# Kernel tuning notes

Hardware: AMD Instinct MI355X
Metric: run time of the kernel (lower is better)

## Reference

```python
import jax, jax.numpy as jnp
import numpy as np

B, T = 64, 256
E = 300          # embedding_size
H = 512          # hidden_num
L = 9            # label_size
V = 30000        # vocab_size
S = 30000        # sentence_size


def setup_inputs() -> dict:
    key = jax.random.key(0)
    ks = jax.random.split(key, 14)
    D = 2 * E
    inp = {
        "text": jax.random.randint(ks[0], (B, T), 0, V, dtype=jnp.int32),
        "sentence": jax.random.randint(ks[1], (B, T), 0, S, dtype=jnp.int32),
        "labels": jax.random.randint(ks[2], (B, T), 0, L, dtype=jnp.int32),
        "word_emb": jax.random.normal(ks[3], (V, E), jnp.float32) * 0.05,
        "sent_emb": jax.random.normal(ks[4], (S, E), jnp.float32) * 0.05,
        "Wk_f": jax.random.normal(ks[5], (D, 4 * H), jnp.float32) / np.sqrt(D).astype(np.float32),
        "Wr_f": jax.random.normal(ks[6], (H, 4 * H), jnp.float32) / np.sqrt(H).astype(np.float32),
        "b_f": jnp.zeros((4 * H,), jnp.float32),
        "Wk_b": jax.random.normal(ks[7], (D, 4 * H), jnp.float32) / np.sqrt(D).astype(np.float32),
        "Wr_b": jax.random.normal(ks[8], (H, 4 * H), jnp.float32) / np.sqrt(H).astype(np.float32),
        "b_b": jnp.zeros((4 * H,), jnp.float32),
        "Wd": jax.random.normal(ks[9], (2 * H, L), jnp.float32) / np.sqrt(2 * H).astype(np.float32),
        "bd": jnp.zeros((L,), jnp.float32),
        "trans": jax.random.uniform(ks[10], (L, L), jnp.float32),
    }
    return inp


def lstm(x, Wk, Wr, b):
    # x: [B,T,D]; Keras LSTM gate order i,f,g,o; sigmoid recurrent act, tanh act.
    xz = jnp.einsum('btd,dk->btk', x, Wk) + b  # one big GEMM for all timesteps
    h0 = jnp.zeros((x.shape[0], Wr.shape[0]), x.dtype)

    def step(carry, z_t):
        h, c = carry
        z = z_t + h @ Wr
        i, f, g, o = jnp.split(z, 4, axis=-1)
        c = jax.nn.sigmoid(f) * c + jax.nn.sigmoid(i) * jnp.tanh(g)
        h = jax.nn.sigmoid(o) * jnp.tanh(c)
        return (h, c), h

    _, hs = jax.lax.scan(step, (h0, h0), jnp.swapaxes(xz, 0, 1))
    return jnp.swapaxes(hs, 0, 1)  # [B,T,H]


def crf_log_likelihood(logits, labels, mask, trans):
    maskf = mask.astype(logits.dtype)
    # unary score of the gold path
    unary = jnp.take_along_axis(logits, labels[..., None], axis=-1)[..., 0]  # [B,T]
    unary = jnp.sum(unary * maskf, axis=-1)
    # binary (transition) score
    binary = trans[labels[:, :-1], labels[:, 1:]]  # [B,T-1]
    binary = jnp.sum(binary * maskf[:, 1:], axis=-1)
    # forward algorithm (log partition), masked steps carry alpha
    logits_tm = jnp.swapaxes(logits, 0, 1)  # [T,B,L]
    mask_tm = jnp.swapaxes(mask, 0, 1)

    def step(alpha, inputs):
        logit_t, m_t = inputs
        new = jax.nn.logsumexp(alpha[:, :, None] + trans[None], axis=1) + logit_t
        return jnp.where(m_t[:, None], new, alpha), None

    alpha, _ = jax.lax.scan(step, logits_tm[0], (logits_tm[1:], mask_tm[1:]))
    log_norm = jax.nn.logsumexp(alpha, axis=-1)
    return unary + binary - log_norm


def crf_decode(logits, trans, mask):
    b, t, l = logits.shape
    logits_tm = jnp.swapaxes(logits, 0, 1)
    mask_tm = jnp.swapaxes(mask, 0, 1)
    ident = jnp.broadcast_to(jnp.arange(l)[None], (b, l))

    def step(alpha, inputs):
        logit_t, m_t = inputs
        score = alpha[:, :, None] + trans[None]      # [B,L,L]
        bp = jnp.argmax(score, axis=1)               # [B,L]
        new = jnp.max(score, axis=1) + logit_t
        alpha = jnp.where(m_t[:, None], new, alpha)
        bp = jnp.where(m_t[:, None], bp, ident)      # identity through padding
        return alpha, bp

    alpha, bps = jax.lax.scan(step, logits_tm[0], (logits_tm[1:], mask_tm[1:]))
    last = jnp.argmax(alpha, axis=-1)  # [B]

    def back(tag, bp):
        prev = jnp.take_along_axis(bp, tag[:, None], axis=1)[:, 0]
        return prev, prev

    _, tags = jax.lax.scan(back, last, bps, reverse=True)  # [T-1,B], original time order
    tags = jnp.concatenate([tags, last[None]], axis=0)     # [T,B]
    return jnp.swapaxes(tags, 0, 1).astype(jnp.int32)


def reference(text, sentence, labels, word_emb, sent_emb, Wk_f, Wr_f, b_f,
              Wk_b, Wr_b, b_b, Wd, bd, trans):
    x = jnp.concatenate([word_emb[text], sent_emb[sentence]], axis=-1)  # [B,T,2E]
    hf = lstm(x, Wk_f, Wr_f, b_f)
    hb = lstm(x[:, ::-1], Wk_b, Wr_b, b_b)[:, ::-1]
    h = jnp.concatenate([hf, hb], axis=-1)  # [B,T,2H]
    logits = h @ Wd + bd                    # [B,T,L]
    text_lens = jnp.sum((text != 0).astype(jnp.int32), axis=-1)
    mask = jnp.arange(T)[None, :] < text_lens[:, None]
    log_likelihood = crf_log_likelihood(logits, labels, mask, trans)
    pred_tags = crf_decode(logits, trans, mask)
    return logits, text_lens, log_likelihood, pred_tags
```

## Files before the change

kernel.cpp:

```cpp
#include <hip/hip_runtime.h>
#include <hip/hip_bf16.h>
#include <math.h>

#define BB 64
#define TT 256
#define EE 300
#define DD 600
#define KP 608
#define HH 512
#define G4 2048
#define LL 9
#define NT (BB*TT)

typedef __attribute__((ext_vector_type(8))) short short8;
typedef __attribute__((ext_vector_type(4))) float floatx4;

#define XZF_OFF  ((size_t)0)
#define XZ_BYTES ((size_t)NT * G4 * 2)
#define XZB_OFF  (XZF_OFF + XZ_BYTES)
#define HSR_OFF  (XZB_OFF + XZ_BYTES)
#define HS_BYTES ((size_t)NT * HH * 2)
#define HSF_OFF  (HSR_OFF)
#define HSB_OFF  (HSR_OFF + HS_BYTES)
#define XG_OFF   (HSR_OFF)
#define WKT_OFF  (HSR_OFF + 19922944)
#define BP_OFF   (HSR_OFF + 25165824)
#define WRT_OFF  (HSR_OFF + (size_t)2 * HS_BYTES)
#define HB_OFF   (WRT_OFF + 4194304)
#define HB_BYTES ((size_t)2 * 2 * BB * HH * 4)
#define LEN_OFF  (HB_OFF + HB_BYTES)

#define OUT_LOGITS 0
#define OUT_LENS   (BB*TT*LL)
#define OUT_LL     (OUT_LENS + BB)
#define OUT_TAGS   (OUT_LL + BB)

__global__ __launch_bounds__(256) void prep_xg(
    const int* __restrict__ text, const int* __restrict__ sent,
    const float* __restrict__ wemb, const float* __restrict__ semb,
    __hip_bfloat16* __restrict__ xg)
{
    int n = blockIdx.x;
    int ti = text[n], si = sent[n];
    __hip_bfloat16* o = xg + (size_t)n * KP;
    for (int k = threadIdx.x; k < KP; k += 256) {
        float v = 0.f;
        if (k < EE)      v = wemb[(size_t)ti * EE + k];
        else if (k < DD) v = semb[(size_t)si * EE + (k - EE)];
        o[k] = __float2bfloat16(v);
    }
}

__global__ __launch_bounds__(256) void transpose_w(
    const float* __restrict__ Wf, const float* __restrict__ Wb,
    __hip_bfloat16* __restrict__ outT, int Din, int Dpad)
{
    int dir = blockIdx.z;
    const float* W = dir ? Wb : Wf;
    __hip_bfloat16* o = outT + (size_t)dir * G4 * Dpad;
    int n0 = blockIdx.x * 64, d0 = blockIdx.y * 64;
    __shared__ float tile[64][65];
    int c = threadIdx.x & 63, r4 = threadIdx.x >> 6;
    #pragma unroll
    for (int rr = 0; rr < 64; rr += 4) {
        int d = d0 + rr + r4;
        tile[rr + r4][c] = (d < Din) ? W[(size_t)d * G4 + n0 + c] : 0.f;
    }
    __syncthreads();
    #pragma unroll
    for (int rr = 0; rr < 64; rr += 4) {
        int n = n0 + rr + r4;
        int d = d0 + c;
        if (d < Dpad) o[(size_t)n * Dpad + d] = __float2bfloat16(tile[c][rr + r4]);
    }
}

__global__ __launch_bounds__(256) void embed_gemm(
    const __hip_bfloat16* __restrict__ xg,
    const __hip_bfloat16* __restrict__ WkT,
    const float* __restrict__ b_f, const float* __restrict__ b_b,
    __hip_bfloat16* __restrict__ xz_f, __hip_bfloat16* __restrict__ xz_b)
{
    int dir = blockIdx.z;
    const __hip_bfloat16* wt = WkT + (size_t)dir * G4 * KP;
    const float* bias = dir ? b_b : b_f;
    __hip_bfloat16* xz = dir ? xz_b : xz_f;

    int n0 = blockIdx.x * 64;
    int c0 = blockIdx.y * 64;
    int wave = threadIdx.x >> 6, lane = threadIdx.x & 63;
    int mt2 = (wave & 1) * 2;
    int nt2 = (wave >> 1) * 2;
    int lm = lane & 15, lk8 = (lane >> 4) * 8;

    const short8* ap[2], *bp[2];
    ap[0] = (const short8*)(xg + (size_t)(n0 + (mt2+0)*16 + lm) * KP + lk8);
    ap[1] = (const short8*)(xg + (size_t)(n0 + (mt2+1)*16 + lm) * KP + lk8);
    bp[0] = (const short8*)(wt + (size_t)(c0 + (nt2+0)*16 + lm) * KP + lk8);
    bp[1] = (const short8*)(wt + (size_t)(c0 + (nt2+1)*16 + lm) * KP + lk8);

    floatx4 acc[2][2] = {};
    for (int kc = 0; kc < KP/32; ++kc) {
        short8 a0 = ap[0][kc*4];
        short8 a1 = ap[1][kc*4];
        short8 b0 = bp[0][kc*4];
        short8 b1 = bp[1][kc*4];
        acc[0][0] = __builtin_amdgcn_mfma_f32_16x16x32_bf16(a0, b0, acc[0][0], 0,0,0);
        acc[0][1] = __builtin_amdgcn_mfma_f32_16x16x32_bf16(a0, b1, acc[0][1], 0,0,0);
        acc[1][0] = __builtin_amdgcn_mfma_f32_16x16x32_bf16(a1, b0, acc[1][0], 0,0,0);
        acc[1][1] = __builtin_amdgcn_mfma_f32_16x16x32_bf16(a1, b1, acc[1][1], 0,0,0);
    }

    float bias0 = bias[c0 + (nt2+0)*16 + lm];
    float bias1 = bias[c0 + (nt2+1)*16 + lm];
    int lr = (lane >> 4) * 4;
    #pragma unroll
    for (int mi = 0; mi < 2; ++mi)
        #pragma unroll
        for (int ni = 0; ni < 2; ++ni) {
            int col = c0 + (nt2+ni)*16 + lm;
            float bs = ni ? bias1 : bias0;
            #pragma unroll
            for (int r = 0; r < 4; ++r) {
                int row = n0 + (mt2+mi)*16 + lr + r;
                xz[(size_t)row * G4 + col] = __float2bfloat16(acc[mi][ni][r] + bs);
            }
        }
}

__global__ __launch_bounds__(256, 1) void lstm_coop(
    const __hip_bfloat16* __restrict__ xz_f, const __hip_bfloat16* __restrict__ xz_b,
    const __hip_bfloat16* __restrict__ WrT,
    unsigned* __restrict__ hbx,
    __hip_bfloat16* __restrict__ hs_f, __hip_bfloat16* __restrict__ hs_b)
{
    int blk = blockIdx.x;
    int dir = blk >> 7, sub = blk & 127;
    int r0 = (sub >> 5) * 16;
    int h0 = (sub & 31) * 16;
    int tid = threadIdx.x;
    int gate = tid >> 6, lane = tid & 63;
    int lm = lane & 15, lk8 = (lane >> 4) * 8;

    const __hip_bfloat16* xz = dir ? xz_b : xz_f;
    __hip_bfloat16* hs = dir ? hs_b : hs_f;
    const __hip_bfloat16* wrt = WrT + (size_t)dir * G4 * HH;
    unsigned* hbd = hbx + (size_t)dir * 2 * BB * HH;

    short8 bfrag[16];
    {
        const short8* wp = (const short8*)(wrt + (size_t)(gate*HH + h0 + lm) * HH + lk8);
        #pragma unroll
        for (int kc = 0; kc < 16; ++kc) bfrag[kc] = wp[kc*4];
    }

    __shared__ unsigned short htile[16][520];
    __shared__ float zbuf[4][16][17];

    int er = tid >> 3, ec = (tid & 7) * 2;
    float c0st = 0.f, c1st = 0.f;

    int zr = (lane >> 4) * 4;

    for (int t = 0; t < TT; ++t) {
        int tok = dir ? (TT - 1 - t) : t;

        float xzv[4];
        #pragma unroll
        for (int r = 0; r < 4; ++r) {
            int n = (r0 + zr + r) * TT + tok;
            xzv[r] = __bfloat162float(xz[(size_t)n * G4 + gate*HH + h0 + lm]);
        }

        unsigned long long v[16];
        {
            const unsigned long long* src = (const unsigned long long*)
                (hbd + (size_t)(t & 1) * BB * HH + (size_t)r0 * HH);
            const unsigned long long pat =
                ((unsigned long long)(unsigned)t << 48) |
                ((unsigned long long)(unsigned)t << 16);
            for (;;) {
                #pragma unroll
                for (int q = 0; q < 16; ++q)
                    v[q] = __hip_atomic_load(src + tid + 256*q,
                            __ATOMIC_RELAXED, __HIP_MEMORY_SCOPE_AGENT);
                unsigned long long bad = 0;
                #pragma unroll
                for (int q = 0; q < 16; ++q)
                    bad |= (v[q] ^ pat) & 0xFFFF0000FFFF0000ULL;
                if (bad == 0) break;
                __builtin_amdgcn_s_sleep(2);
            }
        }
        #pragma unroll
        for (int q = 0; q < 16; ++q) {
            int idx = tid + 256*q;
            int row = idx >> 8, cp = idx & 255;
            unsigned lo = (unsigned)(v[q] & 0xffffu);
            unsigned hi = (unsigned)((v[q] >> 32) & 0xffffu);
            *(unsigned*)&htile[row][cp * 2] = lo | (hi << 16);
        }
        __syncthreads();

        floatx4 acc = {};
        #pragma unroll
        for (int kc = 0; kc < 16; ++kc) {
            short8 a = *(const short8*)&htile[lm][kc * 32 + lk8];
            acc = __builtin_amdgcn_mfma_f32_16x16x32_bf16(a, bfrag[kc], acc, 0,0,0);
        }

        #pragma unroll
        for (int r = 0; r < 4; ++r)
            zbuf[gate][zr + r][lm] = acc[r] + xzv[r];
        __syncthreads();

        if (tid < 128) {
            float zi0 = zbuf[0][er][ec],   zi1 = zbuf[0][er][ec+1];
            float zf0 = zbuf[1][er][ec],   zf1 = zbuf[1][er][ec+1];
            float zg0 = zbuf[2][er][ec],   zg1 = zbuf[2][er][ec+1];
            float zo0 = zbuf[3][er][ec],   zo1 = zbuf[3][er][ec+1];
            float si0 = 1.f/(1.f+__expf(-zi0)), si1 = 1.f/(1.f+__expf(-zi1));
            float sf0 = 1.f/(1.f+__expf(-zf0)), sf1 = 1.f/(1.f+__expf(-zf1));
            float so0 = 1.f/(1.f+__expf(-zo0)), so1 = 1.f/(1.f+__expf(-zo1));
            c0st = sf0 * c0st + si0 * tanhf(zg0);
            c1st = sf1 * c1st + si1 * tanhf(zg1);
            float h0v = so0 * tanhf(c0st);
            float h1v = so1 * tanhf(c1st);
            unsigned u0 = (unsigned)__builtin_bit_cast(unsigned short, __float2bfloat16(h0v));
            unsigned u1 = (unsigned)__builtin_bit_cast(unsigned short, __float2bfloat16(h1v));
            unsigned tg = (unsigned)(t + 1) << 16;
            unsigned long long pay =
                ((unsigned long long)(tg | u1) << 32) | (unsigned long long)(tg | u0);
            __hip_atomic_store(
                (unsigned long long*)(hbd + (size_t)((t+1) & 1) * BB * HH
                                          + (size_t)(r0 + er) * HH + h0 + ec),
                pay, __ATOMIC_RELAXED, __HIP_MEMORY_SCOPE_AGENT);
            *(unsigned*)(hs + ((size_t)(r0 + er) * TT + tok) * HH + h0 + ec) =
                u0 | (u1 << 16);
        }
    }
}

__global__ __launch_bounds__(64) void logits_kernel(
    const __hip_bfloat16* __restrict__ hs_f, const __hip_bfloat16* __restrict__ hs_b,
    const float* __restrict__ Wd, const float* __restrict__ bd,
    float* __restrict__ out)
{
    int n = blockIdx.x;
    int tid = threadIdx.x;
    __shared__ float red[64][10];
    float acc[LL] = {};
    for (int kk = 0; kk < 16; ++kk) {
        int k = kk * 64 + tid;
        float hv = (k < HH) ? __bfloat162float(hs_f[(size_t)n * HH + k])
                            : __bfloat162float(hs_b[(size_t)n * HH + (k - HH)]);
        const float* w = Wd + (size_t)k * LL;
        #pragma unroll
        for (int l = 0; l < LL; ++l) acc[l] += hv * w[l];
    }
    #pragma unroll
    for (int l = 0; l < LL; ++l) red[tid][l] = acc[l];
    __syncthreads();
    for (int s = 32; s > 0; s >>= 1) {
        if (tid < s)
            for (int l = 0; l < LL; ++l) red[tid][l] += red[tid + s][l];
        __syncthreads();
    }
    if (tid < LL) out[(size_t)n * LL + tid] = red[0][tid] + bd[tid];
}

__global__ __launch_bounds__(256) void lens_kernel(
    const int* __restrict__ text, float* __restrict__ out_lens, int* __restrict__ len_i)
{
    int b = blockIdx.x, tid = threadIdx.x;
    __shared__ int sred[256];
    sred[tid] = (text[b * TT + tid] != 0) ? 1 : 0;
    __syncthreads();
    for (int s = 128; s > 0; s >>= 1) {
        if (tid < s) sred[tid] += sred[tid + s];
        __syncthreads();
    }
    if (tid == 0) { out_lens[b] = (float)sred[0]; len_i[b] = sred[0]; }
}

__global__ __launch_bounds__(128) void crf_kernel(
    const float* __restrict__ logits, const int* __restrict__ labels,
    const float* __restrict__ trans, const int* __restrict__ len_i,
    int* __restrict__ bp, float* __restrict__ out_ll, float* __restrict__ out_tags)
{
    int b = blockIdx.x, tid = threadIdx.x;
    int len = len_i[b];
    const float* lg = logits + (size_t)b * TT * LL;
    const int* lab = labels + b * TT;

    __shared__ float tr[81];
    __shared__ float alpha[LL], vit[LL], newa[LL], newv[LL];
    __shared__ int newbp[LL];
    __shared__ float partial[128];

    if (tid < 81) tr[tid] = trans[tid];
    if (tid < LL) { alpha[tid] = lg[tid]; vit[tid] = lg[tid]; }
    __syncthreads();

    float up = 0.f;
    for (int t = tid; t < TT; t += 128) {
        float m = (t < len) ? 1.f : 0.f;
        up += m * lg[t * LL + lab[t]];
        if (t >= 1) up += m * tr[lab[t - 1] * LL + lab[t]];
    }
    partial[tid] = up;
    __syncthreads();
    for (int s = 64; s > 0; s >>= 1) {
        if (tid < s) partial[tid] += partial[tid + s];
        __syncthreads();
    }

    for (int t = 1; t < TT; ++t) {
        bool m = t < len;
        if (tid < LL) {
            int j = tid;
            float mx = -1e30f;
            #pragma unroll
            for (int i = 0; i < LL; ++i) mx = fmaxf(mx, alpha[i] + tr[i * LL + j]);
            float s = 0.f;
            #pragma unroll
            for (int i = 0; i < LL; ++i) s += __expf(alpha[i] + tr[i * LL + j] - mx);
            newa[j] = mx + __logf(s) + lg[t * LL + j];
        } else if (tid >= 64 && tid < 64 + LL) {
            int j = tid - 64;
            float best = -1e30f; int bi = 0;
            #pragma unroll
            for (int i = 0; i < LL; ++i) {
                float sc = vit[i] + tr[i * LL + j];
                if (sc > best) { best = sc; bi = i; }
            }
            newv[j] = best + lg[t * LL + j];
            newbp[j] = bi;
        }
        __syncthreads();
        if (tid < LL) {
            if (m) alpha[tid] = newa[tid];
        } else if (tid >= 64 && tid < 64 + LL) {
            int j = tid - 64;
            if (m) vit[j] = newv[j];
            bp[((size_t)b * (TT - 1) + (t - 1)) * LL + j] = m ? newbp[j] : j;
        }
        __syncthreads();
    }

    if (tid == 0) {
        float mx = -1e30f;
        #pragma unroll
        for (int j = 0; j < LL; ++j) mx = fmaxf(mx, alpha[j]);
        float s = 0.f;
        #pragma unroll
        for (int j = 0; j < LL; ++j) s += __expf(alpha[j] - mx);
        out_ll[b] = partial[0] - (mx + __logf(s));

        float bv = vit[0]; int last = 0;
        #pragma unroll
        for (int j = 1; j < LL; ++j) if (vit[j] > bv) { bv = vit[j]; last = j; }
        out_tags[b * TT + (TT - 1)] = (float)last;
        int tag = last;
        for (int s2 = TT - 2; s2 >= 0; --s2) {
            tag = bp[((size_t)b * (TT - 1) + s2) * LL + tag];
            out_tags[b * TT + s2] = (float)tag;
        }
    }
}

extern "C" void kernel_launch(void* const* d_in, const int* in_sizes, int n_in,
                              void* d_out, int out_size, void* d_ws, size_t ws_size,
                              hipStream_t stream)
{
    const int*   text  = (const int*)d_in[0];
    const int*   sent  = (const int*)d_in[1];
    const int*   labels= (const int*)d_in[2];
    const float* wemb  = (const float*)d_in[3];
    const float* semb  = (const float*)d_in[4];
    const float* Wk_f  = (const float*)d_in[5];
    const float* Wr_f  = (const float*)d_in[6];
    const float* b_f   = (const float*)d_in[7];
    const float* Wk_b  = (const float*)d_in[8];
    const float* Wr_b  = (const float*)d_in[9];
    const float* b_b   = (const float*)d_in[10];
    const float* Wd    = (const float*)d_in[11];
    const float* bd    = (const float*)d_in[12];
    const float* trans = (const float*)d_in[13];
    float* out = (float*)d_out;

    char* ws = (char*)d_ws;
    __hip_bfloat16* xz_f = (__hip_bfloat16*)(ws + XZF_OFF);
    __hip_bfloat16* xz_b = (__hip_bfloat16*)(ws + XZB_OFF);
    __hip_bfloat16* hs_f = (__hip_bfloat16*)(ws + HSF_OFF);
    __hip_bfloat16* hs_b = (__hip_bfloat16*)(ws + HSB_OFF);
    __hip_bfloat16* xg   = (__hip_bfloat16*)(ws + XG_OFF);
    __hip_bfloat16* WkT  = (__hip_bfloat16*)(ws + WKT_OFF);
    __hip_bfloat16* WrT  = (__hip_bfloat16*)(ws + WRT_OFF);
    unsigned*       hbx  = (unsigned*)(ws + HB_OFF);
    int*      bp    = (int*)(ws + BP_OFF);
    int*      leni  = (int*)(ws + LEN_OFF);

    prep_xg <<<NT,  256, 0, stream>>>(text, sent, wemb, semb, xg);
    transpose_w<<<dim3(G4/64, (KP+63)/64, 2), 256, 0, stream>>>(Wk_f, Wk_b, WkT, DD, KP);
    transpose_w<<<dim3(G4/64, HH/64, 2),      256, 0, stream>>>(Wr_f, Wr_b, WrT, HH, HH);
    hipMemsetAsync(ws + HB_OFF, 0, HB_BYTES + 256, stream);

    embed_gemm<<<dim3(NT/64, G4/64, 2), 256, 0, stream>>>(
        xg, WkT, b_f, b_b, xz_f, xz_b);

    {
        void* args[] = { (void*)&xz_f, (void*)&xz_b, (void*)&WrT,
                         (void*)&hbx, (void*)&hs_f, (void*)&hs_b };
        hipLaunchCooperativeKernel((const void*)lstm_coop, dim3(256), dim3(256),
                                   args, 0, stream);
    }

    logits_kernel<<<NT, 64, 0, stream>>>(hs_f, hs_b, Wd, bd, out + OUT_LOGITS);
    lens_kernel<<<BB, 256, 0, stream>>>(text, out + OUT_LENS, leni);
    crf_kernel<<<BB, 128, 0, stream>>>(out + OUT_LOGITS, labels, trans, leni,
                                       bp, out + OUT_LL, out + OUT_TAGS);
}
```

Before: 1.578 ms.

## Add volatile fast-path exchange to LSTM, MFMA logits, fused warp-level CRF

Remaps LSTM blocks so each batch-row group spreads across XCDs by block index, and adds a volatile (non-atomic) fast exchange buffer for the recurrent h that is polled first. After repeated misses it falls back to the existing agent-scope atomic buffer. Widens the embedding GEMM tile to 128 rows per block. Replaces the scalar logits reduction with an MFMA kernel over a bf16-transposed Wd. Fuses lens and CRF into one kernel that keeps logits, transitions and backpointers in LDS and does the forward and Viterbi recursion with wave shuffles instead of block syncs. The volatile path relies on cache coherence behaviour that the code does not guarantee, which adds a correctness risk.

```diff
diff --git a/kernel.cpp b/kernel.cpp
--- a/kernel.cpp
+++ b/kernel.cpp
@@ -24,11 +24,11 @@
 #define HSB_OFF  (HSR_OFF + HS_BYTES)
 #define XG_OFF   (HSR_OFF)
 #define WKT_OFF  (HSR_OFF + 19922944)
-#define BP_OFF   (HSR_OFF + 25165824)
 #define WRT_OFF  (HSR_OFF + (size_t)2 * HS_BYTES)
-#define HB_OFF   (WRT_OFF + 4194304)
-#define HB_BYTES ((size_t)2 * 2 * BB * HH * 4)
-#define LEN_OFF  (HB_OFF + HB_BYTES)
+#define BK_OFF   (WRT_OFF + 4194304)
+#define FAST_OFF (BK_OFF + 524288)
+#define EX_BYTES ((size_t)2 * 2 * BB * HH * 4)
+#define WDT_OFF  XZF_OFF
 
 #define OUT_LOGITS 0
 #define OUT_LENS   (BB*TT*LL)
@@ -75,6 +75,15 @@
     }
 }
 
+__global__ __launch_bounds__(256) void prep_wdT(
+    const float* __restrict__ Wd, __hip_bfloat16* __restrict__ WdT)
+{
+    for (int i = threadIdx.x + blockIdx.x * 256; i < 16 * 1024; i += gridDim.x * 256) {
+        int nn = i >> 10, k = i & 1023;
+        WdT[i] = __float2bfloat16(nn < LL ? Wd[(size_t)k * LL + nn] : 0.f);
+    }
+}
+
 __global__ __launch_bounds__(256) void embed_gemm(
     const __hip_bfloat16* __restrict__ xg,
     const __hip_bfloat16* __restrict__ WkT,
@@ -86,58 +95,64 @@
     const float* bias = dir ? b_b : b_f;
     __hip_bfloat16* xz = dir ? xz_b : xz_f;
 
-    int n0 = blockIdx.x * 64;
+    int n0 = blockIdx.x * 128;
     int c0 = blockIdx.y * 64;
     int wave = threadIdx.x >> 6, lane = threadIdx.x & 63;
-    int mt2 = (wave & 1) * 2;
-    int nt2 = (wave >> 1) * 2;
+    int m0 = (wave & 1) * 64;
+    int nn0 = (wave >> 1) * 32;
     int lm = lane & 15, lk8 = (lane >> 4) * 8;
 
-    const short8* ap[2], *bp[2];
-    ap[0] = (const short8*)(xg + (size_t)(n0 + (mt2+0)*16 + lm) * KP + lk8);
-    ap[1] = (const short8*)(xg + (size_t)(n0 + (mt2+1)*16 + lm) * KP + lk8);
-    bp[0] = (const short8*)(wt + (size_t)(c0 + (nt2+0)*16 + lm) * KP + lk8);
-    bp[1] = (const short8*)(wt + (size_t)(c0 + (nt2+1)*16 + lm) * KP + lk8);
-
-    floatx4 acc[2][2] = {};
+    const short8 *ap[4], *bp2[2];
+    #pragma unroll
+    for (int i = 0; i < 4; ++i)
+        ap[i] = (const short8*)(xg + (size_t)(n0 + m0 + i*16 + lm) * KP + lk8);
+    #pragma unroll
+    for (int i = 0; i < 2; ++i)
+        bp2[i] = (const short8*)(wt + (size_t)(c0 + nn0 + i*16 + lm) * KP + lk8);
+
+    floatx4 acc[4][2] = {};
     for (int kc = 0; kc < KP/32; ++kc) {
-        short8 a0 = ap[0][kc*4];
-        short8 a1 = ap[1][kc*4];
-        short8 b0 = bp[0][kc*4];
-        short8 b1 = bp[1][kc*4];
+        short8 a0 = ap[0][kc*4], a1 = ap[1][kc*4], a2 = ap[2][kc*4], a3 = ap[3][kc*4];
+        short8 b0 = bp2[0][kc*4], b1 = bp2[1][kc*4];
         acc[0][0] = __builtin_amdgcn_mfma_f32_16x16x32_bf16(a0, b0, acc[0][0], 0,0,0);
         acc[0][1] = __builtin_amdgcn_mfma_f32_16x16x32_bf16(a0, b1, acc[0][1], 0,0,0);
         acc[1][0] = __builtin_amdgcn_mfma_f32_16x16x32_bf16(a1, b0, acc[1][0], 0,0,0);
         acc[1][1] = __builtin_amdgcn_mfma_f32_16x16x32_bf16(a1, b1, acc[1][1], 0,0,0);
-    }
-
-    float bias0 = bias[c0 + (nt2+0)*16 + lm];
-    float bias1 = bias[c0 + (nt2+1)*16 + lm];
+        acc[2][0] = __builtin_amdgcn_mfma_f32_16x16x32_bf16(a2, b0, acc[2][0], 0,0,0);
+        acc[2][1] = __builtin_amdgcn_mfma_f32_16x16x32_bf16(a2, b1, acc[2][1], 0,0,0);
+        acc[3][0] = __builtin_amdgcn_mfma_f32_16x16x32_bf16(a3, b0, acc[3][0], 0,0,0);
+        acc[3][1] = __builtin_amdgcn_mfma_f32_16x16x32_bf16(a3, b1, acc[3][1], 0,0,0);
+    }
+
     int lr = (lane >> 4) * 4;
     #pragma unroll
-    for (int mi = 0; mi < 2; ++mi)
-        #pragma unroll
-        for (int ni = 0; ni < 2; ++ni) {
-            int col = c0 + (nt2+ni)*16 + lm;
-            float bs = ni ? bias1 : bias0;
+    for (int ni = 0; ni < 2; ++ni) {
+        int col = c0 + nn0 + ni*16 + lm;
+        float bs = bias[col];
+        #pragma unroll
+        for (int mi = 0; mi < 4; ++mi) {
             #pragma unroll
             for (int r = 0; r < 4; ++r) {
-                int row = n0 + (mt2+mi)*16 + lr + r;
+                int row = n0 + m0 + mi*16 + lr + r;
                 xz[(size_t)row * G4 + col] = __float2bfloat16(acc[mi][ni][r] + bs);
             }
         }
+    }
 }
 
 __global__ __launch_bounds__(256, 1) void lstm_coop(
     const __hip_bfloat16* __restrict__ xz_f, const __hip_bfloat16* __restrict__ xz_b,
     const __hip_bfloat16* __restrict__ WrT,
-    unsigned* __restrict__ hbx,
+    unsigned* __restrict__ bk,
+    unsigned* __restrict__ fast,
     __hip_bfloat16* __restrict__ hs_f, __hip_bfloat16* __restrict__ hs_b)
 {
     int blk = blockIdx.x;
-    int dir = blk >> 7, sub = blk & 127;
-    int r0 = (sub >> 5) * 16;
-    int h0 = (sub & 31) * 16;
+    int g = blk & 7;
+    int member = blk >> 3;
+    int dir = g >> 2;
+    int r0 = (g & 3) * 16;
+    int h0 = member * 16;
     int tid = threadIdx.x;
     int gate = tid >> 6, lane = tid & 63;
     int lm = lane & 15, lk8 = (lane >> 4) * 8;
@@ -145,7 +160,8 @@
     const __hip_bfloat16* xz = dir ? xz_b : xz_f;
     __hip_bfloat16* hs = dir ? hs_b : hs_f;
     const __hip_bfloat16* wrt = WrT + (size_t)dir * G4 * HH;
-    unsigned* hbd = hbx + (size_t)dir * 2 * BB * HH;
+    unsigned* bkd = bk + (size_t)dir * 2 * BB * HH;
+    unsigned* fsd = fast + (size_t)dir * 2 * BB * HH;
 
     short8 bfrag[16];
     {
@@ -159,30 +175,41 @@
 
     int er = tid >> 3, ec = (tid & 7) * 2;
     float c0st = 0.f, c1st = 0.f;
-
     int zr = (lane >> 4) * 4;
+
+    bool fastok = true;
+    int fallcnt = 0;
 
     for (int t = 0; t < TT; ++t) {
         int tok = dir ? (TT - 1 - t) : t;
-
-        float xzv[4];
-        #pragma unroll
-        for (int r = 0; r < 4; ++r) {
-            int n = (r0 + zr + r) * TT + tok;
-            xzv[r] = __bfloat162float(xz[(size_t)n * G4 + gate*HH + h0 + lm]);
-        }
+        size_t soff = (size_t)(t & 1) * BB * HH + (size_t)r0 * HH;
+        const unsigned long long pat =
+            ((unsigned long long)(unsigned)t << 48) |
+            ((unsigned long long)(unsigned)t << 16);
 
         unsigned long long v[16];
-        {
-            const unsigned long long* src = (const unsigned long long*)
-                (hbd + (size_t)(t & 1) * BB * HH + (size_t)r0 * HH);
-            const unsigned long long pat =
-                ((unsigned long long)(unsigned)t << 48) |
-                ((unsigned long long)(unsigned)t << 16);
+        bool got = false;
+        if (fastok) {
+            const volatile unsigned long long* fsrc =
+                (const volatile unsigned long long*)(fsd + soff);
+            for (int spin = 0; spin < 24; ++spin) {
+                unsigned long long bad = 0;
+                #pragma unroll
+                for (int q = 0; q < 16; ++q) v[q] = fsrc[tid + 256*q];
+                #pragma unroll
+                for (int q = 0; q < 16; ++q)
+                    bad |= (v[q] ^ pat) & 0xFFFF0000FFFF0000ULL;
+                if (__all(bad == 0)) { got = true; break; }
+                __builtin_amdgcn_s_sleep(1);
+            }
+            if (!got) { if (++fallcnt >= 8) fastok = false; }
+        }
+        if (!got) {
+            const unsigned long long* bsrc = (const unsigned long long*)(bkd + soff);
             for (;;) {
                 #pragma unroll
                 for (int q = 0; q < 16; ++q)
-                    v[q] = __hip_atomic_load(src + tid + 256*q,
+                    v[q] = __hip_atomic_load(bsrc + tid + 256*q,
                             __ATOMIC_RELAXED, __HIP_MEMORY_SCOPE_AGENT);
                 unsigned long long bad = 0;
                 #pragma unroll
@@ -192,13 +219,19 @@
                 __builtin_amdgcn_s_sleep(2);
             }
         }
+
+        float xzv[4];
+        #pragma unroll
+        for (int r = 0; r < 4; ++r) {
+            int n = (r0 + zr + r) * TT + tok;
+            xzv[r] = __bfloat162float(xz[(size_t)n * G4 + gate*HH + h0 + lm]);
+        }
+
         #pragma unroll
         for (int q = 0; q < 16; ++q) {
-            int idx = tid + 256*q;
-            int row = idx >> 8, cp = idx & 255;
             unsigned lo = (unsigned)(v[q] & 0xffffu);
             unsigned hi = (unsigned)((v[q] >> 32) & 0xffffu);
-            *(unsigned*)&htile[row][cp * 2] = lo | (hi << 16);
+            *(unsigned*)&htile[q][tid * 2] = lo | (hi << 16);
         }
         __syncthreads();
 
@@ -231,142 +264,140 @@
             unsigned tg = (unsigned)(t + 1) << 16;
             unsigned long long pay =
                 ((unsigned long long)(tg | u1) << 32) | (unsigned long long)(tg | u0);
-            __hip_atomic_store(
-                (unsigned long long*)(hbd + (size_t)((t+1) & 1) * BB * HH
-                                          + (size_t)(r0 + er) * HH + h0 + ec),
-                pay, __ATOMIC_RELAXED, __HIP_MEMORY_SCOPE_AGENT);
+            size_t eoff = (size_t)((t+1) & 1) * BB * HH + (size_t)(r0 + er) * HH + h0 + ec;
+            *(volatile unsigned long long*)(fsd + eoff) = pay;
+            __hip_atomic_store((unsigned long long*)(bkd + eoff), pay,
+                               __ATOMIC_RELAXED, __HIP_MEMORY_SCOPE_AGENT);
             *(unsigned*)(hs + ((size_t)(r0 + er) * TT + tok) * HH + h0 + ec) =
                 u0 | (u1 << 16);
         }
     }
 }
 
-__global__ __launch_bounds__(64) void logits_kernel(
+__global__ __launch_bounds__(256) void logits_kernel(
     const __hip_bfloat16* __restrict__ hs_f, const __hip_bfloat16* __restrict__ hs_b,
-    const float* __restrict__ Wd, const float* __restrict__ bd,
+    const __hip_bfloat16* __restrict__ WdT, const float* __restrict__ bd,
     float* __restrict__ out)
 {
-    int n = blockIdx.x;
-    int tid = threadIdx.x;
-    __shared__ float red[64][10];
-    float acc[LL] = {};
-    for (int kk = 0; kk < 16; ++kk) {
-        int k = kk * 64 + tid;
-        float hv = (k < HH) ? __bfloat162float(hs_f[(size_t)n * HH + k])
-                            : __bfloat162float(hs_b[(size_t)n * HH + (k - HH)]);
-        const float* w = Wd + (size_t)k * LL;
-        #pragma unroll
-        for (int l = 0; l < LL; ++l) acc[l] += hv * w[l];
-    }
-    #pragma unroll
-    for (int l = 0; l < LL; ++l) red[tid][l] = acc[l];
-    __syncthreads();
-    for (int s = 32; s > 0; s >>= 1) {
-        if (tid < s)
-            for (int l = 0; l < LL; ++l) red[tid][l] += red[tid + s][l];
-        __syncthreads();
-    }
-    if (tid < LL) out[(size_t)n * LL + tid] = red[0][tid] + bd[tid];
-}
-
-__global__ __launch_bounds__(256) void lens_kernel(
-    const int* __restrict__ text, float* __restrict__ out_lens, int* __restrict__ len_i)
+    int n0 = blockIdx.x * 64;
+    int wave = threadIdx.x >> 6, lane = threadIdx.x & 63;
+    int lm = lane & 15, lk8 = (lane >> 4) * 8;
+    int nw = n0 + wave * 16;
+    const short8* af = (const short8*)(hs_f + (size_t)(nw + lm) * HH + lk8);
+    const short8* ab = (const short8*)(hs_b + (size_t)(nw + lm) * HH + lk8);
+    const short8* bw = (const short8*)(WdT + (size_t)lm * 1024 + lk8);
+    floatx4 acc = {};
+    #pragma unroll
+    for (int kc = 0; kc < 16; ++kc) {
+        acc = __builtin_amdgcn_mfma_f32_16x16x32_bf16(af[kc*4], bw[kc*4], acc, 0,0,0);
+        acc = __builtin_amdgcn_mfma_f32_16x16x32_bf16(ab[kc*4], bw[(kc+16)*4], acc, 0,0,0);
+    }
+    if (lm < LL) {
+        float bv = bd[lm];
+        #pragma unroll
+        for (int r = 0; r < 4; ++r) {
+            int n = nw + (lane >> 4) * 4 + r;
+            out[(size_t)n * LL + lm] = acc[r] + bv;
+        }
+    }
+}
+
+__global__ __launch_bounds__(256) void crf_kernel(
+    const float* __restrict__ logits, const int* __restrict__ text,
+    const int* __restrict__ labels, const float* __restrict__ trans,
+    float* __restrict__ out_lens, float* __restrict__ out_ll,
+    float* __restrict__ out_tags)
 {
     int b = blockIdx.x, tid = threadIdx.x;
-    __shared__ int sred[256];
-    sred[tid] = (text[b * TT + tid] != 0) ? 1 : 0;
+    const float* lg = logits + (size_t)b * TT * LL;
+    const int* lab = labels + b * TT;
+
+    __shared__ float lgs[TT * LL];
+    __shared__ float trs[81];
+    __shared__ unsigned char bps[255 * LL + 1];
+    __shared__ float partial[256];
+    __shared__ int ired[256];
+    __shared__ float tagf[TT];
+
+    for (int i = tid; i < TT * LL; i += 256) lgs[i] = lg[i];
+    if (tid < 81) trs[tid] = trans[tid];
+    ired[tid] = (text[b * TT + tid] != 0) ? 1 : 0;
     __syncthreads();
     for (int s = 128; s > 0; s >>= 1) {
-        if (tid < s) sred[tid] += sred[tid + s];
+        if (tid < s) ired[tid] += ired[tid + s];
         __syncthreads();
     }
-    if (tid == 0) { out_lens[b] = (float)sred[0]; len_i[b] = sred[0]; }
-}
-
-__global__ __launch_bounds__(128) void crf_kernel(
-    const float* __restrict__ logits, const int* __restrict__ labels,
-    const float* __restrict__ trans, const int* __restrict__ len_i,
-    int* __restrict__ bp, float* __restrict__ out_ll, float* __restrict__ out_tags)
-{
-    int b = blockIdx.x, tid = threadIdx.x;
-    int len = len_i[b];
-    const float* lg = logits + (size_t)b * TT * LL;
-    const int* lab = labels + b * TT;
-
-    __shared__ float tr[81];
-    __shared__ float alpha[LL], vit[LL], newa[LL], newv[LL];
-    __shared__ int newbp[LL];
-    __shared__ float partial[128];
-
-    if (tid < 81) tr[tid] = trans[tid];
-    if (tid < LL) { alpha[tid] = lg[tid]; vit[tid] = lg[tid]; }
-    __syncthreads();
+    int len = ired[0];
+    if (tid == 0) out_lens[b] = (float)len;
 
     float up = 0.f;
-    for (int t = tid; t < TT; t += 128) {
+    for (int t = tid; t < TT; t += 256) {
         float m = (t < len) ? 1.f : 0.f;
-        up += m * lg[t * LL + lab[t]];
-        if (t >= 1) up += m * tr[lab[t - 1] * LL + lab[t]];
+        up += m * lgs[t * LL + lab[t]];
+        if (t >= 1) up += m * trs[lab[t - 1] * LL + lab[t]];
     }
     partial[tid] = up;
     __syncthreads();
-    for (int s = 64; s > 0; s >>= 1) {
+    for (int s = 128; s > 0; s >>= 1) {
         if (tid < s) partial[tid] += partial[tid + s];
         __syncthreads();
     }
 
-    for (int t = 1; t < TT; ++t) {
-        bool m = t < len;
-        if (tid < LL) {
-            int j = tid;
+    if (tid < 64) {
+        int lane = tid;
+        int j = (lane < LL) ? lane : 0;
+        float trj[LL];
+        #pragma unroll
+        for (int i = 0; i < LL; ++i) trj[i] = trs[i * LL + j];
+        float alpha = lgs[j];
+        float vit = alpha;
+        for (int t = 1; t < TT; ++t) {
+            bool m = t < len;
+            float lgv = lgs[t * LL + j];
+            float ta[LL];
+            float mx = -1e30f, bv = -1e30f; int bi = 0;
+            #pragma unroll
+            for (int i = 0; i < LL; ++i) {
+                float av = __shfl(alpha, i);
+                float vv = __shfl(vit, i);
+                ta[i] = av + trj[i];
+                mx = fmaxf(mx, ta[i]);
+                float sv = vv + trj[i];
+                if (sv > bv) { bv = sv; bi = i; }
+            }
+            float s = 0.f;
+            #pragma unroll
+            for (int i = 0; i < LL; ++i) s += __expf(ta[i] - mx);
+            float newa = mx + __logf(s) + lgv;
+            float newv = bv + lgv;
+            if (m) { alpha = newa; vit = newv; }
+            if (lane < LL) bps[(t - 1) * LL + lane] = (unsigned char)(m ? bi : lane);
+        }
+        float aX[LL], vX[LL];
+        #pragma unroll
+        for (int i = 0; i < LL; ++i) { aX[i] = __shfl(alpha, i); vX[i] = __shfl(vit, i); }
+        if (lane == 0) {
             float mx = -1e30f;
             #pragma unroll
-            for (int i = 0; i < LL; ++i) mx = fmaxf(mx, alpha[i] + tr[i * LL + j]);
+            for (int i = 0; i < LL; ++i) mx = fmaxf(mx, aX[i]);
             float s = 0.f;
             #pragma unroll
-            for (int i = 0; i < LL; ++i) s += __expf(alpha[i] + tr[i * LL + j] - mx);
-            newa[j] = mx + __logf(s) + lg[t * LL + j];
-        } else if (tid >= 64 && tid < 64 + LL) {
-            int j = tid - 64;
-            float best = -1e30f; int bi = 0;
-            #pragma unroll
-            for (int i = 0; i < LL; ++i) {
-                float sc = vit[i] + tr[i * LL + j];
-                if (sc > best) { best = sc; bi = i; }
+            for (int i = 0; i < LL; ++i) s += __expf(aX[i] - mx);
+            out_ll[b] = partial[0] - (mx + __logf(s));
+
+            float bvv = vX[0]; int last = 0;
+            #pragma unroll
+            for (int i = 1; i < LL; ++i) if (vX[i] > bvv) { bvv = vX[i]; last = i; }
+            tagf[TT - 1] = (float)last;
+            int tg = last;
+            for (int s2 = TT - 2; s2 >= 0; --s2) {
+                tg = bps[s2 * LL + tg];
+                tagf[s2] = (float)tg;
             }
-            newv[j] = best + lg[t * LL + j];
-            newbp[j] = bi;
-        }
-        __syncthreads();
-        if (tid < LL) {
-            if (m) alpha[tid] = newa[tid];
-        } else if (tid >= 64 && tid < 64 + LL) {
-            int j = tid - 64;
-            if (m) vit[j] = newv[j];
-            bp[((size_t)b * (TT - 1) + (t - 1)) * LL + j] = m ? newbp[j] : j;
-        }
-        __syncthreads();
-    }
-
-    if (tid == 0) {
-        float mx = -1e30f;
-        #pragma unroll
-        for (int j = 0; j < LL; ++j) mx = fmaxf(mx, alpha[j]);
-        float s = 0.f;
-        #pragma unroll
-        for (int j = 0; j < LL; ++j) s += __expf(alpha[j] - mx);
-        out_ll[b] = partial[0] - (mx + __logf(s));
-
-        float bv = vit[0]; int last = 0;
-        #pragma unroll
-        for (int j = 1; j < LL; ++j) if (vit[j] > bv) { bv = vit[j]; last = j; }
-        out_tags[b * TT + (TT - 1)] = (float)last;
-        int tag = last;
-        for (int s2 = TT - 2; s2 >= 0; --s2) {
-            tag = bp[((size_t)b * (TT - 1) + s2) * LL + tag];
-            out_tags[b * TT + s2] = (float)tag;
-        }
-    }
+        }
+    }
+    __syncthreads();
+    out_tags[b * TT + tid] = tagf[tid];
 }
 
 extern "C" void kernel_launch(void* const* d_in, const int* in_sizes, int n_in,
@@ -397,27 +428,27 @@
     __hip_bfloat16* xg   = (__hip_bfloat16*)(ws + XG_OFF);
     __hip_bfloat16* WkT  = (__hip_bfloat16*)(ws + WKT_OFF);
     __hip_bfloat16* WrT  = (__hip_bfloat16*)(ws + WRT_OFF);
-    unsigned*       hbx  = (unsigned*)(ws + HB_OFF);
-    int*      bp    = (int*)(ws + BP_OFF);
-    int*      leni  = (int*)(ws + LEN_OFF);
+    unsigned*       bk   = (unsigned*)(ws + BK_OFF);
+    unsigned*       fast = (unsigned*)(ws + FAST_OFF);
+    __hip_bfloat16* WdT  = (__hip_bfloat16*)(ws + WDT_OFF);
 
     prep_xg <<<NT,  256, 0, stream>>>(text, sent, wemb, semb, xg);
     transpose_w<<<dim3(G4/64, (KP+63)/64, 2), 256, 0, stream>>>(Wk_f, Wk_b, WkT, DD, KP);
     transpose_w<<<dim3(G4/64, HH/64, 2),      256, 0, stream>>>(Wr_f, Wr_b, WrT, HH, HH);
-    hipMemsetAsync(ws + HB_OFF, 0, HB_BYTES + 256, stream);
-
-    embed_gemm<<<dim3(NT/64, G4/64, 2), 256, 0, stream>>>(
+    hipMemsetAsync(ws + BK_OFF, 0, 2 * EX_BYTES, stream);
+
+    embed_gemm<<<dim3(NT/128, G4/64, 2), 256, 0, stream>>>(
         xg, WkT, b_f, b_b, xz_f, xz_b);
 
     {
         void* args[] = { (void*)&xz_f, (void*)&xz_b, (void*)&WrT,
-                         (void*)&hbx, (void*)&hs_f, (void*)&hs_b };
+                         (void*)&bk, (void*)&fast, (void*)&hs_f, (void*)&hs_b };
         hipLaunchCooperativeKernel((const void*)lstm_coop, dim3(256), dim3(256),
                                    args, 0, stream);
     }
 
-    logits_kernel<<<NT, 64, 0, stream>>>(hs_f, hs_b, Wd, bd, out + OUT_LOGITS);
-    lens_kernel<<<BB, 256, 0, stream>>>(text, out + OUT_LENS, leni);
-    crf_kernel<<<BB, 128, 0, stream>>>(out + OUT_LOGITS, labels, trans, leni,
-                                       bp, out + OUT_LL, out + OUT_TAGS);
-}
+    prep_wdT<<<16, 256, 0, stream>>>(Wd, WdT);
+    logits_kernel<<<NT/64, 256, 0, stream>>>(hs_f, hs_b, WdT, bd, out + OUT_LOGITS);
+    crf_kernel<<<BB, 256, 0, stream>>>(out + OUT_LOGITS, text, labels, trans,
+                                       out + OUT_LENS, out + OUT_LL, out + OUT_TAGS);
+}
```

Measured after the change: 2.432 ms. +54.1%, slower.
